# Optimization experiments

Measured on AMD Instinct MI355X. Metric: run time of the kernel, lower is better.

The kernel has to match this reference:

```python
import jax, jax.numpy as jnp
import numpy as np

N_NODES = 20000
N_EDGES = 640000
NUM_FEATURES = 128
HIDDEN = 64
HEADS = 4
NUM_CLASSES = 16
NEG_SLOPE = 0.2  # PyG GATConv default leaky_relu slope


def gat_conv(x, src, dst, W, att_s, att_d, b, num_nodes, concat):
    """PyG-style GATConv (inference: attention dropout is identity).
    x: [N, F_in]; src/dst: [E] (self-loops already included);
    W: [F_in, H*C]; att_s/att_d: [H, C]; b: [H*C] or [C]."""
    H, C = att_s.shape
    h = (x @ W).reshape(num_nodes, H, C)            # [N,H,C]
    a_s = jnp.sum(h * att_s, axis=-1)               # [N,H]
    a_d = jnp.sum(h * att_d, axis=-1)               # [N,H]
    e = jax.nn.leaky_relu(a_s[src] + a_d[dst], NEG_SLOPE)  # [E,H]
    # softmax over incoming edges of each destination node
    emax = jax.ops.segment_max(e, dst, num_segments=num_nodes)  # [N,H]
    ex = jnp.exp(e - emax[dst])
    denom = jax.ops.segment_sum(ex, dst, num_segments=num_nodes)
    alpha = ex / denom[dst]                         # [E,H]
    msg = h[src] * alpha[..., None]                 # [E,H,C]
    out = jax.ops.segment_sum(msg, dst, num_segments=num_nodes)  # [N,H,C]
    out = out.reshape(num_nodes, H * C) if concat else out.mean(axis=1)
    return out + b


def setup_inputs() -> dict:
    key = jax.random.key(0)
    ks = jax.random.split(key, 12)
    d1_in, d1_out = NUM_FEATURES, HEADS * HIDDEN
    d2_in, d2_out = HEADS * HIDDEN, HEADS * HIDDEN
    return {
        "x": jax.random.normal(ks[0], (N_NODES, NUM_FEATURES), dtype=jnp.float32),
        "edge_index": jax.random.randint(ks[1], (2, N_EDGES), 0, N_NODES, dtype=jnp.int64)
        if jax.config.jax_enable_x64 else
        jax.random.randint(ks[1], (2, N_EDGES), 0, N_NODES, dtype=jnp.int32),
        "W1": jax.random.normal(ks[2], (d1_in, d1_out), dtype=jnp.float32) / np.sqrt(d1_in),
        "att_src1": jax.random.normal(ks[3], (HEADS, HIDDEN), dtype=jnp.float32) / np.sqrt(HIDDEN),
        "att_dst1": jax.random.normal(ks[4], (HEADS, HIDDEN), dtype=jnp.float32) / np.sqrt(HIDDEN),
        "b1": jnp.zeros((HEADS * HIDDEN,), dtype=jnp.float32),
        "W2": jax.random.normal(ks[5], (d2_in, d2_out), dtype=jnp.float32) / np.sqrt(d2_in),
        "att_src2": jax.random.normal(ks[6], (HEADS, HIDDEN), dtype=jnp.float32) / np.sqrt(HIDDEN),
        "att_dst2": jax.random.normal(ks[7], (HEADS, HIDDEN), dtype=jnp.float32) / np.sqrt(HIDDEN),
        "b2": jnp.zeros((HIDDEN,), dtype=jnp.float32),
        "Wout": jax.random.normal(ks[8], (HIDDEN, NUM_CLASSES), dtype=jnp.float32) / np.sqrt(HIDDEN),
        "bout": jnp.zeros((NUM_CLASSES,), dtype=jnp.float32),
    }


def reference(x, edge_index, W1, att_src1, att_dst1, b1, W2, att_src2, att_dst2, b2, Wout, bout):
    N = x.shape[0]
    loops = jnp.arange(N, dtype=edge_index.dtype)
    src = jnp.concatenate([edge_index[0], loops])   # PyG add_self_loops=True
    dst = jnp.concatenate([edge_index[1], loops])
    h = gat_conv(x, src, dst, W1, att_src1, att_dst1, b1, N, concat=True)
    h = jax.nn.elu(h)                               # dropout is identity at eval
    h = gat_conv(h, src, dst, W2, att_src2, att_dst2, b2, N, concat=False)
    return h @ Wout + bout
```

## Files before the change

### kernel.cpp

```cpp
#include <hip/hip_runtime.h>
#include <hip/hip_bf16.h>
#include <hip/hip_fp16.h>


#define HEADS 4
#define CDIM 64
#define HC 256
#define ELLW 96
#define CNTS 16
#define NCHUNK 320

typedef __attribute__((ext_vector_type(8))) short bf16x8;
typedef __attribute__((ext_vector_type(4))) float f32x4;

__device__ __forceinline__ short f32_to_bf16_rne(float v) {
  unsigned u = __float_as_uint(v);
  unsigned r = (u + 0x7FFFu + ((u >> 16) & 1u)) >> 16;
  return (short)r;
}
__device__ __forceinline__ float bf16_bits_to_f32(short s) {
  return __uint_as_float(((unsigned)(unsigned short)s) << 16);
}

__device__ __forceinline__ void fma_mix2(float& alo, float& ahi,
                                         unsigned reg, float ex) {
  asm("v_fma_mix_f32 %0, %2, %3, %0 op_sel:[0,0,0] op_sel_hi:[1,0,0]\n\t"
      "v_fma_mix_f32 %1, %2, %3, %1 op_sel:[1,0,0] op_sel_hi:[1,0,0]"
      : "+v"(alo), "+v"(ahi)
      : "v"(reg), "v"(ex));
}

__global__ __launch_bounds__(256) void pack_w12_kernel(
    const float* __restrict__ W1, short* __restrict__ W1h,
    short* __restrict__ W1l, const float* __restrict__ W2,
    short* __restrict__ W2h, short* __restrict__ W2l,
    int* __restrict__ cnt, int N) {
  const int i = blockIdx.x * 256 + threadIdx.x;
  if (i < N) cnt[i * CNTS] = 0;
  if (i < 128 * 256) {
    const int k = i >> 8, n = i & 255;
    const float v = W1[i];
    const short hi = f32_to_bf16_rne(v);
    W1h[n * 128 + k] = hi;
    W1l[n * 128 + k] = f32_to_bf16_rne(v - bf16_bits_to_f32(hi));
  } else {
    const int j = i - 128 * 256;
    if (j >= 256 * 256) return;
    const int k = j >> 8, n = j & 255;
    const float v = W2[j];
    const short hi = f32_to_bf16_rne(v);
    W2h[n * 256 + k] = hi;
    W2l[n * 256 + k] = f32_to_bf16_rne(v - bf16_bits_to_f32(hi));
  }
}

__global__ __launch_bounds__(256) void gemm_mfma_split(
    const float* __restrict__ A, const short* __restrict__ Wt_hi,
    const short* __restrict__ Wt_lo, __half* __restrict__ h16,
    const float* __restrict__ att_s, const float* __restrict__ att_d,
    float* __restrict__ a_s, float* __restrict__ a_d, int M, int K) {
  __shared__ alignas(16) short As_hi[64 * 32];
  __shared__ alignas(16) short As_lo[64 * 32];
  const int t = threadIdx.x;
  const int wave = t >> 6;
  const int lane = t & 63;
  const int quad = lane >> 4;
  const int m16 = lane & 15;
  const int row0 = blockIdx.x * 64;
  const int col0 = wave * 64;
  const int head = wave;

  f32x4 acc[4][4] = {};

  for (int k0 = 0; k0 < K; k0 += 32) {
    if (k0) __syncthreads();
    {
      const int r = t >> 2, seg = t & 3;
      const int gr = row0 + r;
      float vv[8] = {0.f, 0.f, 0.f, 0.f, 0.f, 0.f, 0.f, 0.f};
      if (gr < M) {
        const float* ap = A + (size_t)gr * K + k0 + seg * 8;
        const float4 v0 = *(const float4*)ap;
        const float4 v1 = *(const float4*)(ap + 4);
        vv[0] = v0.x; vv[1] = v0.y; vv[2] = v0.z; vv[3] = v0.w;
        vv[4] = v1.x; vv[5] = v1.y; vv[6] = v1.z; vv[7] = v1.w;
      }
      bf16x8 h8, l8;
#pragma unroll
      for (int j = 0; j < 8; ++j) {
        const short hi = f32_to_bf16_rne(vv[j]);
        h8[j] = hi;
        l8[j] = f32_to_bf16_rne(vv[j] - bf16_bits_to_f32(hi));
      }
      *(bf16x8*)(As_hi + r * 32 + seg * 8) = h8;
      *(bf16x8*)(As_lo + r * 32 + seg * 8) = l8;
    }
    bf16x8 b_hi[4], b_lo[4];
#pragma unroll
    for (int nt = 0; nt < 4; ++nt) {
      const size_t off = (size_t)(col0 + nt * 16 + m16) * K + k0 + quad * 8;
      b_hi[nt] = *(const bf16x8*)(Wt_hi + off);
      b_lo[nt] = *(const bf16x8*)(Wt_lo + off);
    }
    __syncthreads();
    bf16x8 a_hi[4], a_lo[4];
#pragma unroll
    for (int mt = 0; mt < 4; ++mt) {
      const int off = (mt * 16 + m16) * 32 + quad * 8;
      a_hi[mt] = *(const bf16x8*)(As_hi + off);
      a_lo[mt] = *(const bf16x8*)(As_lo + off);
    }
#pragma unroll
    for (int mt = 0; mt < 4; ++mt)
#pragma unroll
      for (int nt = 0; nt < 4; ++nt) {
        acc[mt][nt] = __builtin_amdgcn_mfma_f32_16x16x32_bf16(
            a_hi[mt], b_hi[nt], acc[mt][nt], 0, 0, 0);
        acc[mt][nt] = __builtin_amdgcn_mfma_f32_16x16x32_bf16(
            a_hi[mt], b_lo[nt], acc[mt][nt], 0, 0, 0);
        acc[mt][nt] = __builtin_amdgcn_mfma_f32_16x16x32_bf16(
            a_lo[mt], b_hi[nt], acc[mt][nt], 0, 0, 0);
      }
  }
  float sa[4], da[4];
#pragma unroll
  for (int nt = 0; nt < 4; ++nt) {
    sa[nt] = att_s[col0 + nt * 16 + m16];
    da[nt] = att_d[col0 + nt * 16 + m16];
  }
#pragma unroll
  for (int mt = 0; mt < 4; ++mt)
#pragma unroll
    for (int r = 0; r < 4; ++r) {
      const int gr = row0 + mt * 16 + quad * 4 + r;
      float ps = acc[mt][0][r] * sa[0] + acc[mt][1][r] * sa[1] +
                 acc[mt][2][r] * sa[2] + acc[mt][3][r] * sa[3];
      float pd = acc[mt][0][r] * da[0] + acc[mt][1][r] * da[1] +
                 acc[mt][2][r] * da[2] + acc[mt][3][r] * da[3];
#pragma unroll
      for (int off = 1; off <= 8; off <<= 1) {
        ps += __shfl_xor(ps, off);
        pd += __shfl_xor(pd, off);
      }
      if (gr < M) {
        if (m16 == 0) {
          a_s[gr * HEADS + head] = ps;
          a_d[gr * HEADS + head] = pd;
        }
#pragma unroll
        for (int nt = 0; nt < 4; ++nt)
          h16[(size_t)gr * HC + col0 + nt * 16 + m16] =
              __float2half(acc[mt][nt][r]);
      }
    }
}

__global__ __launch_bounds__(256) void ell_scatter_kernel(
    const int* __restrict__ src, const int* __restrict__ dst,
    int* __restrict__ cnt, int* __restrict__ ell, int E_raw, int Etot,
    int chunk_sz) {
  const int g = blockIdx.x & 7;
  const int e0 = (blockIdx.x >> 3) * chunk_sz;
  int e1 = e0 + chunk_sz;
  if (e1 > Etot) e1 = Etot;
  for (int e = e0 + threadIdx.x; e < e1; e += 256) {
    const int d = (e < E_raw) ? dst[e] : (e - E_raw);
    if (((d >> 8) & 7) != g) continue;
    const int s = (e < E_raw) ? src[e] : (e - E_raw);
    const int pos = atomicAdd(&cnt[d * CNTS], 1);
    if (pos < ELLW) ell[d * ELLW + pos] = s;
  }
}

__global__ __launch_bounds__(256) void gat_aggregate_kernel(
    const int* __restrict__ cnt, const int* __restrict__ ell,
    const __half* __restrict__ h16, const float* __restrict__ a_s,
    const float* __restrict__ a_d, const float* __restrict__ b,
    float* __restrict__ out, int N, int mode) {
  const int nn = __builtin_amdgcn_readfirstlane(
      blockIdx.x * 4 + (threadIdx.x >> 6));
  if (nn >= N) return;
  const int lane = threadIdx.x & 63;
  const int hd = lane >> 4;
  const float ad = a_d[nn * HEADS + hd];
  const int deg = __builtin_amdgcn_readfirstlane(cnt[nn * CNTS]);
  const int* __restrict__ rowp = ell + nn * ELLW;
  const unsigned nclamp = (unsigned)(N - 1);
  const char* __restrict__ hby = (const char*)h16;
  const unsigned lo8 = (unsigned)lane * 8u;
  float acc0 = 0.f, acc1 = 0.f, acc2 = 0.f, acc3 = 0.f, den = 0.f;

  for (int j0 = 0; j0 < deg; j0 += 8) {
    unsigned su[8];
#pragma unroll
    for (int j = 0; j < 8; ++j) {
      const unsigned s = (unsigned)rowp[j0 + j];
      su[j] = (s > nclamp) ? nclamp : s;
    }
    float asv[8];
    uint2 hv[8];
#pragma unroll
    for (int j = 0; j < 8; ++j) {
      asv[j] = a_s[su[j] * HEADS + hd];
      hv[j] = *(const uint2*)(hby + (((size_t)su[j]) << 9) + lo8);
    }
#pragma unroll
    for (int j = 0; j < 8; ++j) {
      float a = asv[j] + ad;
      a = fmaxf(a, 0.2f * a);
      const float ex = (j0 + j < deg) ? __expf(a) : 0.f;
      den += ex;
      fma_mix2(acc0, acc1, hv[j].x, ex);
      fma_mix2(acc2, acc3, hv[j].y, ex);
    }
  }

  const float inv = 1.f / den;
  float u0 = acc0 * inv, u1 = acc1 * inv, u2 = acc2 * inv, u3 = acc3 * inv;
  if (mode == 0) {
    const float4 bb = *(const float4*)(b + lane * 4);
    u0 += bb.x; u1 += bb.y; u2 += bb.z; u3 += bb.w;
    u0 = (u0 > 0.f) ? u0 : (__expf(u0) - 1.f);
    u1 = (u1 > 0.f) ? u1 : (__expf(u1) - 1.f);
    u2 = (u2 > 0.f) ? u2 : (__expf(u2) - 1.f);
    u3 = (u3 > 0.f) ? u3 : (__expf(u3) - 1.f);
  }
  *(float4*)(out + (size_t)nn * HC + lane * 4) = make_float4(u0, u1, u2, u3);
}

__global__ __launch_bounds__(256) void final_fused_kernel(
    const float* __restrict__ agg, const float* __restrict__ b2,
    const float* __restrict__ Wout, const float* __restrict__ bout,
    float* __restrict__ out, int N) {
  const int n = blockIdx.x * 4 + (threadIdx.x >> 6);
  const int c = threadIdx.x & 63;
  if (n >= N) return;
  const float* ar = agg + (size_t)n * HC;
  const float m = 0.25f * (ar[c] + ar[c + 64] + ar[c + 128] + ar[c + 192]) +
                  b2[c];
  const float4* wr = (const float4*)(Wout + c * 16);
  const float4 w0 = wr[0], w1 = wr[1], w2 = wr[2], w3 = wr[3];
  float p[16] = {m * w0.x, m * w0.y, m * w0.z, m * w0.w,
                 m * w1.x, m * w1.y, m * w1.z, m * w1.w,
                 m * w2.x, m * w2.y, m * w2.z, m * w2.w,
                 m * w3.x, m * w3.y, m * w3.z, m * w3.w};
#pragma unroll
  for (int off = 1; off < 64; off <<= 1)
#pragma unroll
    for (int j = 0; j < 16; ++j) p[j] += __shfl_xor(p[j], off);
  if (c == 0) {
    float* op = out + (size_t)n * 16;
    *(float4*)op = make_float4(p[0] + bout[0], p[1] + bout[1],
                               p[2] + bout[2], p[3] + bout[3]);
    *(float4*)(op + 4) = make_float4(p[4] + bout[4], p[5] + bout[5],
                                     p[6] + bout[6], p[7] + bout[7]);
    *(float4*)(op + 8) = make_float4(p[8] + bout[8], p[9] + bout[9],
                                     p[10] + bout[10], p[11] + bout[11]);
    *(float4*)(op + 12) = make_float4(p[12] + bout[12], p[13] + bout[13],
                                      p[14] + bout[14], p[15] + bout[15]);
  }
}

extern "C" void kernel_launch(void* const* d_in, const int* in_sizes, int n_in,
                              void* d_out, int out_size, void* d_ws, size_t ws_size,
                              hipStream_t stream) {
  const float* x      = (const float*)d_in[0];
  const int*   eidx   = (const int*)d_in[1];
  const float* W1     = (const float*)d_in[2];
  const float* att_s1 = (const float*)d_in[3];
  const float* att_d1 = (const float*)d_in[4];
  const float* b1     = (const float*)d_in[5];
  const float* W2     = (const float*)d_in[6];
  const float* att_s2 = (const float*)d_in[7];
  const float* att_d2 = (const float*)d_in[8];
  const float* b2     = (const float*)d_in[9];
  const float* Wout   = (const float*)d_in[10];
  const float* bout   = (const float*)d_in[11];
  float* out          = (float*)d_out;

  const int N     = in_sizes[0] / 128;
  const int E_raw = in_sizes[1] / 2;
  const int Etot  = E_raw + N;
  const int* src = eidx;
  const int* dst = eidx + E_raw;

  float* ws = (float*)d_ws;
  float* buf_agg = ws;
  float* buf_as  = buf_agg + (size_t)N * HC;
  float* buf_ad  = buf_as + (size_t)N * HEADS;
  __half* h16    = (__half*)(buf_ad + (size_t)N * HEADS);
  int* cnt  = (int*)(h16 + (size_t)N * HC);
  int* ell  = cnt + (size_t)N * CNTS;
  uintptr_t wp = ((uintptr_t)(ell + (size_t)N * ELLW) + 15) & ~(uintptr_t)15;
  short* wt1_hi = (short*)wp;
  short* wt1_lo = wt1_hi + 256 * 128;
  short* wt2_hi = wt1_lo + 256 * 128;
  short* wt2_lo = wt2_hi + 256 * 256;

  const dim3 blk(256);
  const int chunk_sz = (Etot + NCHUNK - 1) / NCHUNK;
  const int g_gemm = (N + 63) / 64;
  const int g_agg = (N + 3) / 4;

  pack_w12_kernel<<<(384 * 256 + 255) / 256, blk, 0, stream>>>(
      W1, wt1_hi, wt1_lo, W2, wt2_hi, wt2_lo, cnt, N);
  ell_scatter_kernel<<<NCHUNK * 8, blk, 0, stream>>>(src, dst, cnt, ell,
                                                     E_raw, Etot, chunk_sz);

  gemm_mfma_split<<<g_gemm, blk, 0, stream>>>(
      x, wt1_hi, wt1_lo, h16, att_s1, att_d1, buf_as, buf_ad, N, 128);
  gat_aggregate_kernel<<<g_agg, blk, 0, stream>>>(cnt, ell, h16, buf_as,
                                                  buf_ad, b1, buf_agg, N, 0);

  gemm_mfma_split<<<g_gemm, blk, 0, stream>>>(
      buf_agg, wt2_hi, wt2_lo, h16, att_s2, att_d2, buf_as, buf_ad, N, 256);
  gat_aggregate_kernel<<<g_agg, blk, 0, stream>>>(cnt, ell, h16, buf_as,
                                                  buf_ad, b2, buf_agg, N, 1);

  final_fused_kernel<<<(N + 3) / 4, blk, 0, stream>>>(buf_agg, b2, Wout, bout,
                                                      out, N);
}
```

Before: 255.3 us.

## Fuse output projection into layer-2 aggregation and use sentinel-padded ELL rows

New measurement: 273.0 us. 1.07x slower.

```diff
diff --git a/kernel.cpp b/kernel.cpp
--- a/kernel.cpp
+++ b/kernel.cpp
@@ -34,9 +34,18 @@
     const float* __restrict__ W1, short* __restrict__ W1h,
     short* __restrict__ W1l, const float* __restrict__ W2,
     short* __restrict__ W2h, short* __restrict__ W2l,
-    int* __restrict__ cnt, int N) {
+    int* __restrict__ cnt, int* __restrict__ ell, __half* __restrict__ h16,
+    float* __restrict__ a_s, int N) {
   const int i = blockIdx.x * 256 + threadIdx.x;
   if (i < N) cnt[i * CNTS] = 0;
+  {
+    int4 dv; dv.x = N; dv.y = N; dv.z = N; dv.w = N;
+    int4* e4 = (int4*)ell;
+    const int tot4 = N * (ELLW / 4);
+    for (int k = i; k < tot4; k += 384 * 256) e4[k] = dv;
+  }
+  if (i < HC) h16[(size_t)N * HC + i] = __float2half(0.f);
+  if (i < HEADS) a_s[N * HEADS + i] = -1e30f;
   if (i < 128 * 256) {
     const int k = i >> 8, n = i & 255;
     const float v = W1[i];
@@ -176,6 +185,7 @@
     const int* __restrict__ cnt, const int* __restrict__ ell,
     const __half* __restrict__ h16, const float* __restrict__ a_s,
     const float* __restrict__ a_d, const float* __restrict__ b,
+    const float* __restrict__ Wout, const float* __restrict__ bout,
     float* __restrict__ out, int N, int mode) {
   const int nn = __builtin_amdgcn_readfirstlane(
       blockIdx.x * 4 + (threadIdx.x >> 6));
@@ -185,7 +195,6 @@
   const float ad = a_d[nn * HEADS + hd];
   const int deg = __builtin_amdgcn_readfirstlane(cnt[nn * CNTS]);
   const int* __restrict__ rowp = ell + nn * ELLW;
-  const unsigned nclamp = (unsigned)(N - 1);
   const char* __restrict__ hby = (const char*)h16;
   const unsigned lo8 = (unsigned)lane * 8u;
   float acc0 = 0.f, acc1 = 0.f, acc2 = 0.f, acc3 = 0.f, den = 0.f;
@@ -195,7 +204,7 @@
 #pragma unroll
     for (int j = 0; j < 8; ++j) {
       const unsigned s = (unsigned)rowp[j0 + j];
-      su[j] = (s > nclamp) ? nclamp : s;
+      su[j] = (s > (unsigned)N) ? (unsigned)N : s;
     }
     float asv[8];
     uint2 hv[8];
@@ -208,7 +217,7 @@
     for (int j = 0; j < 8; ++j) {
       float a = asv[j] + ad;
       a = fmaxf(a, 0.2f * a);
-      const float ex = (j0 + j < deg) ? __expf(a) : 0.f;
+      const float ex = __expf(a);
       den += ex;
       fma_mix2(acc0, acc1, hv[j].x, ex);
       fma_mix2(acc2, acc3, hv[j].y, ex);
@@ -224,40 +233,46 @@
     u1 = (u1 > 0.f) ? u1 : (__expf(u1) - 1.f);
     u2 = (u2 > 0.f) ? u2 : (__expf(u2) - 1.f);
     u3 = (u3 > 0.f) ? u3 : (__expf(u3) - 1.f);
-  }
-  *(float4*)(out + (size_t)nn * HC + lane * 4) = make_float4(u0, u1, u2, u3);
-}
-
-__global__ __launch_bounds__(256) void final_fused_kernel(
-    const float* __restrict__ agg, const float* __restrict__ b2,
-    const float* __restrict__ Wout, const float* __restrict__ bout,
-    float* __restrict__ out, int N) {
-  const int n = blockIdx.x * 4 + (threadIdx.x >> 6);
-  const int c = threadIdx.x & 63;
-  if (n >= N) return;
-  const float* ar = agg + (size_t)n * HC;
-  const float m = 0.25f * (ar[c] + ar[c + 64] + ar[c + 128] + ar[c + 192]) +
-                  b2[c];
-  const float4* wr = (const float4*)(Wout + c * 16);
-  const float4 w0 = wr[0], w1 = wr[1], w2 = wr[2], w3 = wr[3];
-  float p[16] = {m * w0.x, m * w0.y, m * w0.z, m * w0.w,
-                 m * w1.x, m * w1.y, m * w1.z, m * w1.w,
-                 m * w2.x, m * w2.y, m * w2.z, m * w2.w,
-                 m * w3.x, m * w3.y, m * w3.z, m * w3.w};
-#pragma unroll
-  for (int off = 1; off < 64; off <<= 1)
-#pragma unroll
-    for (int j = 0; j < 16; ++j) p[j] += __shfl_xor(p[j], off);
-  if (c == 0) {
-    float* op = out + (size_t)n * 16;
-    *(float4*)op = make_float4(p[0] + bout[0], p[1] + bout[1],
-                               p[2] + bout[2], p[3] + bout[3]);
-    *(float4*)(op + 4) = make_float4(p[4] + bout[4], p[5] + bout[5],
-                                     p[6] + bout[6], p[7] + bout[7]);
-    *(float4*)(op + 8) = make_float4(p[8] + bout[8], p[9] + bout[9],
-                                     p[10] + bout[10], p[11] + bout[11]);
-    *(float4*)(op + 12) = make_float4(p[12] + bout[12], p[13] + bout[13],
-                                      p[14] + bout[14], p[15] + bout[15]);
+    *(float4*)(out + (size_t)nn * HC + lane * 4) = make_float4(u0, u1, u2, u3);
+  } else {
+    u0 += __shfl_xor(u0, 16); u0 += __shfl_xor(u0, 32);
+    u1 += __shfl_xor(u1, 16); u1 += __shfl_xor(u1, 32);
+    u2 += __shfl_xor(u2, 16); u2 += __shfl_xor(u2, 32);
+    u3 += __shfl_xor(u3, 16); u3 += __shfl_xor(u3, 32);
+    const int g16 = lane & 15;
+    const float4 bb = *(const float4*)(b + g16 * 4);
+    float mq[4];
+    mq[0] = 0.25f * u0 + bb.x;
+    mq[1] = 0.25f * u1 + bb.y;
+    mq[2] = 0.25f * u2 + bb.z;
+    mq[3] = 0.25f * u3 + bb.w;
+    float p[16] = {0.f, 0.f, 0.f, 0.f, 0.f, 0.f, 0.f, 0.f,
+                   0.f, 0.f, 0.f, 0.f, 0.f, 0.f, 0.f, 0.f};
+#pragma unroll
+    for (int k = 0; k < 4; ++k) {
+      const float4* rw = (const float4*)(Wout + (g16 * 4 + k) * 16);
+      const float4 w0 = rw[0], w1 = rw[1], w2 = rw[2], w3 = rw[3];
+      const float mk = mq[k];
+      p[0] += mk * w0.x;  p[1] += mk * w0.y;  p[2] += mk * w0.z;  p[3] += mk * w0.w;
+      p[4] += mk * w1.x;  p[5] += mk * w1.y;  p[6] += mk * w1.z;  p[7] += mk * w1.w;
+      p[8] += mk * w2.x;  p[9] += mk * w2.y;  p[10] += mk * w2.z; p[11] += mk * w2.w;
+      p[12] += mk * w3.x; p[13] += mk * w3.y; p[14] += mk * w3.z; p[15] += mk * w3.w;
+    }
+#pragma unroll
+    for (int off = 1; off <= 8; off <<= 1)
+#pragma unroll
+      for (int j = 0; j < 16; ++j) p[j] += __shfl_xor(p[j], off);
+    if (lane == 0) {
+      float* op = out + (size_t)nn * 16;
+      *(float4*)op = make_float4(p[0] + bout[0], p[1] + bout[1],
+                                 p[2] + bout[2], p[3] + bout[3]);
+      *(float4*)(op + 4) = make_float4(p[4] + bout[4], p[5] + bout[5],
+                                       p[6] + bout[6], p[7] + bout[7]);
+      *(float4*)(op + 8) = make_float4(p[8] + bout[8], p[9] + bout[9],
+                                       p[10] + bout[10], p[11] + bout[11]);
+      *(float4*)(op + 12) = make_float4(p[12] + bout[12], p[13] + bout[13],
+                                        p[14] + bout[14], p[15] + bout[15]);
+    }
   }
 }
 
@@ -287,9 +302,9 @@
   float* ws = (float*)d_ws;
   float* buf_agg = ws;
   float* buf_as  = buf_agg + (size_t)N * HC;
-  float* buf_ad  = buf_as + (size_t)N * HEADS;
+  float* buf_ad  = buf_as + (size_t)(N + 1) * HEADS;
   __half* h16    = (__half*)(buf_ad + (size_t)N * HEADS);
-  int* cnt  = (int*)(h16 + (size_t)N * HC);
+  int* cnt  = (int*)(h16 + (size_t)(N + 1) * HC);
   int* ell  = cnt + (size_t)N * CNTS;
   uintptr_t wp = ((uintptr_t)(ell + (size_t)N * ELLW) + 15) & ~(uintptr_t)15;
   short* wt1_hi = (short*)wp;
@@ -302,21 +317,18 @@
   const int g_gemm = (N + 63) / 64;
   const int g_agg = (N + 3) / 4;
 
-  pack_w12_kernel<<<(384 * 256 + 255) / 256, blk, 0, stream>>>(
-      W1, wt1_hi, wt1_lo, W2, wt2_hi, wt2_lo, cnt, N);
+  pack_w12_kernel<<<384, blk, 0, stream>>>(
+      W1, wt1_hi, wt1_lo, W2, wt2_hi, wt2_lo, cnt, ell, h16, buf_as, N);
   ell_scatter_kernel<<<NCHUNK * 8, blk, 0, stream>>>(src, dst, cnt, ell,
                                                      E_raw, Etot, chunk_sz);
 
   gemm_mfma_split<<<g_gemm, blk, 0, stream>>>(
       x, wt1_hi, wt1_lo, h16, att_s1, att_d1, buf_as, buf_ad, N, 128);
-  gat_aggregate_kernel<<<g_agg, blk, 0, stream>>>(cnt, ell, h16, buf_as,
-                                                  buf_ad, b1, buf_agg, N, 0);
+  gat_aggregate_kernel<<<g_agg, blk, 0, stream>>>(
+      cnt, ell, h16, buf_as, buf_ad, b1, Wout, bout, buf_agg, N, 0);
 
   gemm_mfma_split<<<g_gemm, blk, 0, stream>>>(
       buf_agg, wt2_hi, wt2_lo, h16, att_s2, att_d2, buf_as, buf_ad, N, 256);
-  gat_aggregate_kernel<<<g_agg, blk, 0, stream>>>(cnt, ell, h16, buf_as,
-                                                  buf_ad, b2, buf_agg, N, 1);
-
-  final_fused_kernel<<<(N + 3) / 4, blk, 0, stream>>>(buf_agg, b2, Wout, bout,
-                                                      out, N);
-}
+  gat_aggregate_kernel<<<g_agg, blk, 0, stream>>>(
+      cnt, ell, h16, buf_as, buf_ad, b2, Wout, bout, out, N, 1);
+}
```
